# Optimization experiments

Hardware: AMD Instinct MI355X
Metric: run time of the kernel (lower is better)

Reference implementation:

```python
import jax, jax.numpy as jnp
import numpy as np

B = 1_000_000
H = 64
TARGET = 0.62562059 * 10.0  # self.target * scale
# GRN constants from NETC_high.__init__
A1, A2, B1C, B2C, K, NEXP, S, SCALE = 1.0, 1.0, 0.2, 0.2, 1.1, 2, 0.5, 10.0


def setup_inputs() -> dict:
    key = jax.random.key(0)
    ks = jax.random.split(key, 10)
    def xavier(k, shape):
        fan_in, fan_out = shape[1], shape[0]
        std = (2.0 / (fan_in + fan_out)) ** 0.5
        return std * jax.random.normal(k, shape, dtype=jnp.float32)
    return {
        "x": jax.random.uniform(ks[0], (B,), dtype=jnp.float32) * 10.0,
        "y": jax.random.uniform(ks[1], (B,), dtype=jnp.float32) * 10.0,
        "e_x": 0.1 * jax.random.normal(ks[2], (B,), dtype=jnp.float32),
        "e_y": 0.1 * jax.random.normal(ks[3], (B,), dtype=jnp.float32),
        "W1": xavier(ks[4], (H, 2)),
        "b1": jnp.zeros((H,), dtype=jnp.float32),
        "W2": xavier(ks[5], (H, H)),
        "b2": jnp.zeros((H,), dtype=jnp.float32),
        "W3": xavier(ks[6], (1, H)),
        "b3": jnp.zeros((1,), dtype=jnp.float32),
    }


def _mlp(z, W1, b1, W2, b2, W3, b3):
    # ControlNet.function: Linear->ReLU->Linear->ReLU->Linear
    h = jax.nn.relu(z @ W1.T + b1)
    h = jax.nn.relu(h @ W2.T + b2)
    return h @ W3.T + b3  # [*, 1]


def _control(inp, W1, b1, W2, b2, W3, b3):
    # ControlNet.forward: u(x) - u(target)
    tgt = jnp.full((1, 2), TARGET, dtype=inp.dtype)
    return _mlp(inp, W1, b1, W2, b2, W3, b3) - _mlp(tgt, W1, b1, W2, b2, W3, b3)


def reference(x, y, e_x, e_y, W1, b1, W2, b2, W3, b3):
    inp = jnp.stack([x + e_x, y + e_y], axis=-1)  # [B, 2]
    u = _control(inp, W1, b1, W2, b2, W3, b3)[:, 0]  # [B]
    xs = x / SCALE
    ys = y / SCALE
    s2 = S ** NEXP
    hx = xs ** NEXP / (s2 + xs ** NEXP)   # Hill activation in x
    hy = ys ** NEXP / (s2 + ys ** NEXP)
    gx = s2 / (s2 + xs ** NEXP)           # Hill repression by x
    gy = s2 / (s2 + ys ** NEXP)
    dx = SCALE * (A1 * hx + B1C * gy - K * xs + u * hx)
    dy = SCALE * (A2 * hy + B2C * gx - K * ys)
    return (dx, dy, -dx, -dy)
```

## Files before the change

### kernel.cpp

```cpp
#include <hip/hip_runtime.h>

#define BTOT 1000000
#define NCHUNK (BTOT / 64)

typedef _Float16 f16;
typedef f16 f16x2 __attribute__((ext_vector_type(2)));
typedef f16 f16x8 __attribute__((ext_vector_type(8)));
typedef float f32x2 __attribute__((ext_vector_type(2)));
typedef float f32x4 __attribute__((ext_vector_type(4)));

#define WS_BFRAG 16
#define WS_W1A   8208
#define WS_W1B   10256
#define WS_B1P   12304
#define WS_W3V   14352
#define WS_B2V   15376

template<int CTRL>
__device__ __forceinline__ float dpp_add(float v) {
    int pv = __builtin_amdgcn_update_dpp(0, __builtin_bit_cast(int, v),
                                         CTRL, 0xF, 0xF, true);
    return v + __builtin_bit_cast(float, pv);
}
__device__ __forceinline__ float row_reduce16(float p) {
    p = dpp_add<0x128>(p);
    p = dpp_add<0x124>(p);
    p = dpp_add<0x122>(p);
    p = dpp_add<0x121>(p);
    return p;
}

__global__ __launch_bounds__(256) void setup_kernel(
    const float* __restrict__ W1, const float* __restrict__ b1,
    const float* __restrict__ W2, const float* __restrict__ b2,
    const float* __restrict__ W3, unsigned char* __restrict__ ws)
{
    const int tid  = threadIdx.x;
    const int quad = (tid & 63) >> 4;
    const int nl   = tid & 15;

    __shared__ float w2s[64 * 65];
    __shared__ float h1s[64];
    __shared__ float part[4 * 64];

    const float4* W2v = (const float4*)W2;
    #pragma unroll
    for (int r = 0; r < 4; ++r) {
        int idx = r * 256 + tid;
        float4 f = W2v[idx];
        int g = idx * 4, row = g >> 6, col = g & 63;
        float* p = &w2s[row * 65 + col];
        p[0] = f.x; p[1] = f.y; p[2] = f.z; p[3] = f.w;
    }
    const float T = 6.2562059f;
    if (tid < 64)
        h1s[tid] = fmaxf(0.f, W1[2 * tid] * T + W1[2 * tid + 1] * T + b1[tid]);
    __syncthreads();

    {
        int r = tid & 63, kq = tid >> 6;
        float p = 0.f;
        #pragma unroll
        for (int k = 0; k < 16; ++k)
            p = fmaf(w2s[r * 65 + kq * 16 + k], h1s[kq * 16 + k], p);
        part[kq * 64 + r] = p;
    }
    __syncthreads();
    if (tid < 64) {
        float h2 = b2[tid] + part[tid] + part[64 + tid] + part[128 + tid] + part[192 + tid];
        float pr = fmaxf(0.f, h2) * W3[tid];
        #pragma unroll
        for (int m = 1; m < 64; m <<= 1) pr += __shfl_xor(pr, m, 64);
        if (tid == 0) *(float*)ws = pr;
    }

    if (tid < 64) {
        f16x8* bfragT = (f16x8*)(ws + WS_BFRAG);
        #pragma unroll
        for (int n = 0; n < 4; ++n)
            #pragma unroll
            for (int ks = 0; ks < 2; ++ks) {
                f16x8 f;
                #pragma unroll
                for (int j = 0; j < 8; ++j)
                    f[j] = (f16)w2s[(n * 16 + nl) * 65 + ks * 32 + quad * 8 + j];
                bfragT[(n * 2 + ks) * 64 + tid] = f;
            }
        f16x2* w1aT = (f16x2*)(ws + WS_W1A);
        f16x2* w1bT = (f16x2*)(ws + WS_W1B);
        f16x2* b1pT = (f16x2*)(ws + WS_B1P);
        #pragma unroll
        for (int i = 0; i < 8; ++i) {
            int kk = (i < 4) ? (quad * 8 + 2 * i) : (32 + quad * 8 + 2 * (i - 4));
            w1aT[i * 64 + tid] = f16x2{(f16)W1[2 * kk],     (f16)W1[2 * kk + 2]};
            w1bT[i * 64 + tid] = f16x2{(f16)W1[2 * kk + 1], (f16)W1[2 * kk + 3]};
            b1pT[i * 64 + tid] = f16x2{(f16)b1[kk],         (f16)b1[kk + 1]};
        }
        float* w3vT = (float*)(ws + WS_W3V);
        float* b2vT = (float*)(ws + WS_B2V);
        #pragma unroll
        for (int n = 0; n < 4; ++n) {
            w3vT[n * 64 + tid] = W3[n * 16 + nl];
            b2vT[n * 64 + tid] = b2[n * 16 + nl];
        }
    }
}

__global__ __launch_bounds__(256, 4) void netc_kernel(
    const float* __restrict__ x,  const float* __restrict__ y,
    const float* __restrict__ ex, const float* __restrict__ ey,
    const unsigned char* __restrict__ ws,
    float* __restrict__ out)
{
    const int tid  = threadIdx.x;
    const int lane = tid & 63;
    const int wv   = tid >> 6;
    const int quad = lane >> 4;
    const int nl   = lane & 15;

    const float u_tgt = *(const float*)ws;
    const float one_minus_ut = 1.0f - u_tgt;
    const f16x8* bfragT = (const f16x8*)(ws + WS_BFRAG);
    f16x8 bfrag[4][2];
    #pragma unroll
    for (int n = 0; n < 4; ++n)
        #pragma unroll
        for (int ks = 0; ks < 2; ++ks)
            bfrag[n][ks] = bfragT[(n * 2 + ks) * 64 + lane];
    const f16x2* w1aT = (const f16x2*)(ws + WS_W1A);
    const f16x2* w1bT = (const f16x2*)(ws + WS_W1B);
    const f16x2* b1pT = (const f16x2*)(ws + WS_B1P);
    f16x2 w1a[8], w1b[8], b1p[8];
    #pragma unroll
    for (int i = 0; i < 8; ++i) {
        w1a[i] = w1aT[i * 64 + lane];
        w1b[i] = w1bT[i * 64 + lane];
        b1p[i] = b1pT[i * 64 + lane];
    }
    const float* w3vT = (const float*)(ws + WS_W3V);
    const float* b2vT = (const float*)(ws + WS_B2V);
    float w3v[4], b2v[4];
    #pragma unroll
    for (int n = 0; n < 4; ++n) { w3v[n] = w3vT[n * 64 + lane]; b2v[n] = b2vT[n * 64 + lane]; }

    const f16x2 zero2 = {(f16)0.f, (f16)0.f};
    const int srcb = (((nl >> 2) << 4) + quad * 4 + (nl & 3)) << 2;

    const int b  = blockIdx.x;
    const int sb = (b * NCHUNK) >> 10;
    const int se = ((b + 1) * NCHUNK) >> 10;
    int c0 = sb + wv;

    float axv = 0.f, ayv = 0.f, aexv = 0.f, aeyv = 0.f;
    float bxv = 0.f, byv = 0.f, bexv = 0.f, beyv = 0.f;
    if (c0 < se)     { int e = (c0 << 6) + lane;       axv = x[e]; ayv = y[e]; aexv = ex[e]; aeyv = ey[e]; }
    if (c0 + 4 < se) { int e = ((c0 + 4) << 6) + lane; bxv = x[e]; byv = y[e]; bexv = ex[e]; beyv = ey[e]; }

    auto body = [&](int c, float& rx, float& ry, float& rex, float& rey) {
        int e = (c << 6) + lane;
        float cx = rx, cy = ry, cex = rex, cey = rey;
        int pc = c + 8;
        if (pc < se) {
            int pe = (pc << 6) + lane;
            rx = x[pe]; ry = y[pe]; rex = ex[pe]; rey = ey[pe];
        }

        float av = cx + cex, bv = cy + cey;
        f16x2 pab = {(f16)av, (f16)bv};
        int pv = __builtin_bit_cast(int, pab);

        float xs = cx * 0.1f, ys = cy * 0.1f;
        float x2 = xs * xs, y2 = ys * ys;
        float invx = __fdividef(1.0f, 0.25f + x2);
        float invy = __fdividef(1.0f, 0.25f + y2);
        float hx = x2 * invx, hy = y2 * invy;
        float gx = 0.25f * invx, gy = 0.25f * invy;
        float cdx = 10.f * hx;
        float base_dx = fmaf(cdx, one_minus_ut, fmaf(2.f, gy, -11.f * xs));
        float dy = fmaf(10.f, hy, fmaf(2.f, gx, -11.f * ys));
        out[BTOT + e]     = dy;
        out[3 * BTOT + e] = -dy;

        f16x2 pt[4];
        #pragma unroll
        for (int t = 0; t < 4; ++t)
            pt[t] = __builtin_bit_cast(f16x2,
                __builtin_amdgcn_ds_bpermute((t * 16 + nl) << 2, pv));

        float ur[4];
        #pragma unroll
        for (int t = 0; t < 4; ++t) {
            f32x4 acc[4];
            #pragma unroll
            for (int n = 0; n < 4; ++n)
                acc[n] = f32x4{b2v[n], b2v[n], b2v[n], b2v[n]};

            f16x2 a2 = {pt[t][0], pt[t][0]};
            f16x2 bb = {pt[t][1], pt[t][1]};
            union { f16x2 h2[8]; f16x8 fr[2]; } u;
            #pragma unroll
            for (int i = 0; i < 8; ++i) {
                f16x2 h = a2 * w1a[i] + (bb * w1b[i] + b1p[i]);
                u.h2[i] = __builtin_elementwise_max(h, zero2);
            }
            #pragma unroll
            for (int n = 0; n < 4; ++n) {
                acc[n] = __builtin_amdgcn_mfma_f32_16x16x32_f16(u.fr[0], bfrag[n][0], acc[n], 0, 0, 0);
                acc[n] = __builtin_amdgcn_mfma_f32_16x16x32_f16(u.fr[1], bfrag[n][1], acc[n], 0, 0, 0);
            }

            f32x2 p01 = {0.f, 0.f}, p23 = {0.f, 0.f};
            #pragma unroll
            for (int n = 0; n < 4; ++n) {
                f32x2 lo = {acc[n][0], acc[n][1]};
                f32x2 hi = {acc[n][2], acc[n][3]};
                lo = __builtin_elementwise_max(lo, f32x2{0.f, 0.f});
                hi = __builtin_elementwise_max(hi, f32x2{0.f, 0.f});
                f32x2 w = {w3v[n], w3v[n]};
                p01 += lo * w;
                p23 += hi * w;
            }
            float u0 = row_reduce16(p01[0]);
            float u1 = row_reduce16(p01[1]);
            float u2 = row_reduce16(p23[0]);
            float u3 = row_reduce16(p23[1]);
            float v01 = (nl & 1) ? u1 : u0;
            float v23 = (nl & 1) ? u3 : u2;
            ur[t] = (nl & 2) ? v23 : v01;
        }

        float s01  = (nl & 4) ? ur[1] : ur[0];
        float s23  = (nl & 4) ? ur[3] : ur[2];
        float send = (nl & 8) ? s23 : s01;
        float u_raw = __builtin_bit_cast(float,
            __builtin_amdgcn_ds_bpermute(srcb, __builtin_bit_cast(int, send)));

        float dx = fmaf(cdx, u_raw, base_dx);
        out[e]            = dx;
        out[2 * BTOT + e] = -dx;
    };

    for (int c = c0; c < se; c += 8) {
        body(c, axv, ayv, aexv, aeyv);
        if (c + 4 < se)
            body(c + 4, bxv, byv, bexv, beyv);
    }
}

extern "C" void kernel_launch(void* const* d_in, const int* in_sizes, int n_in,
                              void* d_out, int out_size, void* d_ws, size_t ws_size,
                              hipStream_t stream) {
    const float* x  = (const float*)d_in[0];
    const float* y  = (const float*)d_in[1];
    const float* ex = (const float*)d_in[2];
    const float* ey = (const float*)d_in[3];
    const float* W1 = (const float*)d_in[4];
    const float* b1 = (const float*)d_in[5];
    const float* W2 = (const float*)d_in[6];
    const float* b2 = (const float*)d_in[7];
    const float* W3 = (const float*)d_in[8];
    float* out = (float*)d_out;
    unsigned char* ws = (unsigned char*)d_ws;

    setup_kernel<<<1, 256, 0, stream>>>(W1, b1, W2, b2, W3, ws);
    netc_kernel<<<1024, 256, 0, stream>>>(x, y, ex, ey, ws, out);
}
```

Baseline: 106.3 us.

## Stride chunks across waves and issue all input loads before weight setup

The per-block contiguous chunk loop with its two-slot register prefetch is replaced. Each wave now handles up to four chunks strided by 4096 waves across the whole grid. All x/y/e_x/e_y loads for those chunks are issued at kernel start, before the weight-fragment loads, so their latency overlaps the setup and the MLP work. This raises memory-level parallelism and removes the loop-carried prefetch, at the cost of 16 more live registers per lane and a fixed chunk-to-wave mapping that assumes the launch grid matches.

```diff
diff --git a/kernel.cpp b/kernel.cpp
--- a/kernel.cpp
+++ b/kernel.cpp
@@ -118,6 +118,20 @@
     const int quad = lane >> 4;
     const int nl   = lane & 15;
 
+    const int w  = (blockIdx.x << 2) + wv;
+    const int e0 = (w << 6) + lane;
+    const int estep = 4096 << 6;
+
+    float vx[4], vy[4], vex[4], vey[4];
+    #pragma unroll
+    for (int k = 0; k < 4; ++k) {
+        vx[k] = 0.f; vy[k] = 0.f; vex[k] = 0.f; vey[k] = 0.f;
+        if (w + k * 4096 < NCHUNK) {
+            int e = e0 + k * estep;
+            vx[k] = x[e]; vy[k] = y[e]; vex[k] = ex[e]; vey[k] = ey[e];
+        }
+    }
+
     const float u_tgt = *(const float*)ws;
     const float one_minus_ut = 1.0f - u_tgt;
     const f16x8* bfragT = (const f16x8*)(ws + WS_BFRAG);
@@ -146,26 +160,13 @@
     const f16x2 zero2 = {(f16)0.f, (f16)0.f};
     const int srcb = (((nl >> 2) << 4) + quad * 4 + (nl & 3)) << 2;
 
-    const int b  = blockIdx.x;
-    const int sb = (b * NCHUNK) >> 10;
-    const int se = ((b + 1) * NCHUNK) >> 10;
-    int c0 = sb + wv;
-
-    float axv = 0.f, ayv = 0.f, aexv = 0.f, aeyv = 0.f;
-    float bxv = 0.f, byv = 0.f, bexv = 0.f, beyv = 0.f;
-    if (c0 < se)     { int e = (c0 << 6) + lane;       axv = x[e]; ayv = y[e]; aexv = ex[e]; aeyv = ey[e]; }
-    if (c0 + 4 < se) { int e = ((c0 + 4) << 6) + lane; bxv = x[e]; byv = y[e]; bexv = ex[e]; beyv = ey[e]; }
-
-    auto body = [&](int c, float& rx, float& ry, float& rex, float& rey) {
-        int e = (c << 6) + lane;
-        float cx = rx, cy = ry, cex = rex, cey = rey;
-        int pc = c + 8;
-        if (pc < se) {
-            int pe = (pc << 6) + lane;
-            rx = x[pe]; ry = y[pe]; rex = ex[pe]; rey = ey[pe];
-        }
-
-        float av = cx + cex, bv = cy + cey;
+    #pragma unroll
+    for (int k = 0; k < 4; ++k) {
+        if (w + k * 4096 >= NCHUNK) break;
+        const int e = e0 + k * estep;
+        const float cx = vx[k], cy = vy[k];
+
+        float av = cx + vex[k], bv = cy + vey[k];
         f16x2 pab = {(f16)av, (f16)bv};
         int pv = __builtin_bit_cast(int, pab);
 
@@ -216,9 +217,9 @@
                 f32x2 hi = {acc[n][2], acc[n][3]};
                 lo = __builtin_elementwise_max(lo, f32x2{0.f, 0.f});
                 hi = __builtin_elementwise_max(hi, f32x2{0.f, 0.f});
-                f32x2 w = {w3v[n], w3v[n]};
-                p01 += lo * w;
-                p23 += hi * w;
+                f32x2 wq = {w3v[n], w3v[n]};
+                p01 += lo * wq;
+                p23 += hi * wq;
             }
             float u0 = row_reduce16(p01[0]);
             float u1 = row_reduce16(p01[1]);
@@ -238,12 +239,6 @@
         float dx = fmaf(cdx, u_raw, base_dx);
         out[e]            = dx;
         out[2 * BTOT + e] = -dx;
-    };
-
-    for (int c = c0; c < se; c += 8) {
-        body(c, axv, ayv, aexv, aeyv);
-        if (c + 4 < se)
-            body(c + 4, bxv, byv, bexv, beyv);
     }
 }
 
```

New measurement: 103.7 us. 1.02x faster.
